# Kernel tuning notes

Measured on AMD Instinct MI355X. Metric: run time of the kernel, lower is better.

Reference implementation:

```python
import jax, jax.numpy as jnp
import numpy as np

B, S, E = 1, 2048, 2048
H = 16            # num_q_heads
DN = 128          # qk_nope_head_dim
DR = 64           # qk_rope_head_dim
DV = 128          # v_head_dim
R = 512           # kv_lora_rank
QLR = 1536        # q_lora_rank
EPS = 1e-6
ROPE_BASE = 10000.0


def _rmsnorm(x, w):
    var = jnp.mean(jnp.square(x), axis=-1, keepdims=True)
    return x * jax.lax.rsqrt(var + EPS) * w


def _rope_cos_sin(seqlen):
    inv_freq = 1.0 / (ROPE_BASE ** (jnp.arange(0, DR, 2, dtype=jnp.float32) / DR))
    ang = jnp.arange(seqlen, dtype=jnp.float32)[:, None] * inv_freq[None, :]  # [S, DR/2]
    cos = jnp.concatenate([jnp.cos(ang), jnp.cos(ang)], axis=-1)  # [S, DR]
    sin = jnp.concatenate([jnp.sin(ang), jnp.sin(ang)], axis=-1)
    return cos, sin


def _rotate_half(x):
    x1, x2 = jnp.split(x, 2, axis=-1)
    return jnp.concatenate([-x2, x1], axis=-1)


def setup_inputs() -> dict:
    key = jax.random.key(0)
    ks = jax.random.split(key, 8)
    sd = lambda fan_in: 1.0 / np.sqrt(fan_in)
    return {
        "x": jax.random.normal(ks[0], (B, S, E), jnp.float32),
        "w_q_a": jax.random.normal(ks[1], (E, QLR), jnp.float32) * sd(E),
        "q_a_ln_w": jnp.ones((QLR,), jnp.float32),
        "w_q_b": jax.random.normal(ks[2], (QLR, H * (DN + DR)), jnp.float32) * sd(QLR),
        "w_kv_a": jax.random.normal(ks[3], (E, R + DR), jnp.float32) * sd(E),
        "kv_a_ln_w": jnp.ones((R,), jnp.float32),
        "w_kv_b": jax.random.normal(ks[4], (R, H * (DN + DV)), jnp.float32) * sd(R),
        "w_o": jax.random.normal(ks[5], (H * DV, E), jnp.float32) * sd(H * DV),
    }


def reference(x, w_q_a, q_a_ln_w, w_q_b, w_kv_a, kv_a_ln_w, w_kv_b, w_o):
    b, s, _ = x.shape
    # --- low-rank query projection: q_a -> RMSNorm -> q_b ---
    q_a = _rmsnorm(x @ w_q_a, q_a_ln_w)                      # [b,s,QLR]
    q = (q_a @ w_q_b).reshape(b, s, H, DN + DR)               # [b,s,H,192]
    q_nope, q_pe = q[..., :DN], q[..., DN:]
    # --- compressed KV projection (MQA, single KV head) ---
    ckv_kpe = x @ w_kv_a                                      # [b,s,R+DR]
    ckv = _rmsnorm(ckv_kpe[..., :R], kv_a_ln_w)               # [b,s,R]
    k_pe = ckv_kpe[..., R:].reshape(b, s, 1, DR)              # [b,s,1,DR]
    # --- partial RoPE on the rope sub-dims only ---
    cos, sin = _rope_cos_sin(s)
    cos, sin = cos[None, :, None, :], sin[None, :, None, :]
    q_pe = q_pe * cos + _rotate_half(q_pe) * sin
    k_pe = k_pe * cos + _rotate_half(k_pe) * sin
    # --- weight absorption: fold W_uk into q, W_uv @ W_o into output ---
    w_kv = w_kv_b.reshape(R, H, DN + DV)
    w_uk = w_kv[..., :DN]                                     # [R,H,DN]
    w_uv = w_kv[..., DN:]                                     # [R,H,DV]
    w_o3 = w_o.reshape(H, DV, E)
    w_o_abs = jnp.einsum('rhd,hde->hre', w_uv, w_o3)          # [H,R,E]
    q_abs = jnp.einsum('bshd,rhd->bshr', q_nope, w_uk)        # [b,s,H,R]
    # --- attention in compressed (ckv + rope) space ---
    q_full = jnp.concatenate([q_abs, q_pe], axis=-1)          # [b,s,H,R+DR]
    k_full = jnp.concatenate([ckv, k_pe[:, :, 0, :]], axis=-1)  # [b,s,R+DR]
    sm_scale = (DN + DR) ** -0.5
    scores = jnp.einsum('bqhd,bkd->bhqk', q_full, k_full) * sm_scale
    causal = jnp.tril(jnp.ones((s, s), dtype=bool))
    scores = jnp.where(causal[None, None], scores, jnp.finfo(scores.dtype).min)
    attn = jax.nn.softmax(scores, axis=-1)
    o_ckv = jnp.einsum('bhqk,bkr->bqhr', attn, ckv)           # [b,s,H,R]
    # --- absorbed output projection, summed over heads ---
    y = jnp.einsum('bqhr,hre->bqe', o_ckv, w_o_abs)           # [b,s,E]
    return y
```

## Files before the change

### kernel.cpp

```cpp
#include <hip/hip_runtime.h>
#include <math.h>


typedef unsigned short u16;
typedef unsigned int u32;
typedef __bf16 bf16x8 __attribute__((ext_vector_type(8)));
typedef float f32x4 __attribute__((ext_vector_type(4)));

__device__ __forceinline__ u16 f2b(float f) {
  u32 u = __float_as_uint(f);
  u += 0x7FFFu + ((u >> 16) & 1u);
  return (u16)(u >> 16);
}
__device__ __forceinline__ float b2f(u16 v) {
  return __uint_as_float(((u32)v) << 16);
}

#define GLDS(g, l) __builtin_amdgcn_global_load_lds( \
    (const __attribute__((address_space(1))) u32*)(g), \
    (__attribute__((address_space(3))) u32*)(l), 16, 0, 0)

#define MFMA(a, b, c) __builtin_amdgcn_mfma_f32_16x16x32_bf16(a, b, c, 0, 0, 0)

template<int N>
__device__ __forceinline__ void vm_barrier() {
  __builtin_amdgcn_s_waitcnt(0xF70 | N);
  __builtin_amdgcn_s_barrier();
}

__device__ __forceinline__ float block_sum(float v, float* red) {
#pragma unroll
  for (int off = 32; off > 0; off >>= 1) v += __shfl_down(v, off);
  const int lane = threadIdx.x & 63, w = threadIdx.x >> 6;
  if (lane == 0) red[w] = v;
  __syncthreads();
  float r = red[0] + red[1] + red[2] + red[3];
  __syncthreads();
  return r;
}

template<int OUTK>
__global__ __launch_bounds__(256) void gemm_mfma(
    const u16* __restrict__ A, const u16* __restrict__ B, void* __restrict__ Cv,
    int K, int lda, int ldb, int ldc, long sA, long sB, long sC)
{
  __shared__ u16 At[3][4096];
  __shared__ u16 Bt[3][4096];
  const u16* Ab = A + (long)blockIdx.z * sA;
  const u16* Bb = B + (long)blockIdx.z * sB;
  const int tid = threadIdx.x;
  const int w = tid >> 6, lane = tid & 63;
  const int m0 = blockIdx.y * 128, n0 = blockIdx.x * 128;
  const int wm = (w >> 1) * 64, wn = (w & 1) * 64;
  const int fr = lane & 15, fq = lane >> 4;

  const int c0 = w * 2, c1 = w * 2 + 1;
  const int e0 = (c0 * 64 + lane) * 8, e1 = (c1 * 64 + lane) * 8;
  const int r0 = e0 >> 5, col0 = e0 & 31;
  const int r1 = e1 >> 5, col1 = e1 & 31;

  const int nk = K >> 5;
  auto issue = [&](int kc) {
    const int k0 = kc * 32;
    u16* at = At[kc % 3];
    u16* bt = Bt[kc % 3];
    GLDS(Ab + (long)(m0 + r0) * lda + k0 + col0, at + c0 * 512);
    GLDS(Bb + (long)(n0 + r0) * ldb + k0 + col0, bt + c0 * 512);
    GLDS(Ab + (long)(m0 + r1) * lda + k0 + col1, at + c1 * 512);
    GLDS(Bb + (long)(n0 + r1) * ldb + k0 + col1, bt + c1 * 512);
  };

  f32x4 acc[4][4] = {};
  issue(0);
  issue(1);
  vm_barrier<4>();
  for (int kc = 0; kc < nk; ++kc) {
    if (kc + 2 < nk) issue(kc + 2);
    const u16* at = At[kc % 3];
    const u16* bt = Bt[kc % 3];
    bf16x8 af[4], bfr[4];
#pragma unroll
    for (int i = 0; i < 4; ++i)
      af[i] = *(const bf16x8*)(at + (wm + i * 16 + fr) * 32 + fq * 8);
#pragma unroll
    for (int j = 0; j < 4; ++j)
      bfr[j] = *(const bf16x8*)(bt + (wn + j * 16 + fr) * 32 + fq * 8);
#pragma unroll
    for (int i = 0; i < 4; ++i)
#pragma unroll
      for (int j = 0; j < 4; ++j)
        acc[i][j] = MFMA(af[i], bfr[j], acc[i][j]);
    if (kc + 1 < nk) {
      if (kc + 2 < nk) vm_barrier<4>();
      else vm_barrier<0>();
    }
  }

  if (OUTK == 0) {
    float* C = (float*)Cv + (long)blockIdx.z * sC;
#pragma unroll
    for (int i = 0; i < 4; ++i)
#pragma unroll
      for (int j = 0; j < 4; ++j) {
        long base = (long)(m0 + wm + i * 16 + fq * 4) * ldc + (n0 + wn + j * 16 + fr);
#pragma unroll
        for (int r = 0; r < 4; ++r) C[base + (long)r * ldc] = acc[i][j][r];
      }
  } else if (OUTK == 1) {
    u16* C = (u16*)Cv + (long)blockIdx.z * sC;
#pragma unroll
    for (int i = 0; i < 4; ++i)
#pragma unroll
      for (int j = 0; j < 4; ++j) {
        long base = (long)(m0 + wm + i * 16 + fq * 4) * ldc + (n0 + wn + j * 16 + fr);
#pragma unroll
        for (int r = 0; r < 4; ++r) C[base + (long)r * ldc] = f2b(acc[i][j][r]);
      }
  } else {
    u16* C = (u16*)Cv + (long)blockIdx.z * sC;
#pragma unroll
    for (int i = 0; i < 4; ++i)
#pragma unroll
      for (int j = 0; j < 4; ++j) {
        ushort4 v = { f2b(acc[i][j][0]), f2b(acc[i][j][1]),
                      f2b(acc[i][j][2]), f2b(acc[i][j][3]) };
        *(ushort4*)(C + (long)(n0 + wn + j * 16 + fr) * ldc + (m0 + wm + i * 16 + fq * 4)) = v;
      }
  }
}

__global__ __launch_bounds__(256, 2) void attn_flash2(
    const u16* __restrict__ qfb,
    const u16* __restrict__ kfb,
    const u16* __restrict__ vallT,
    u16* __restrict__ ovb)
{
  __shared__ u16 Ks[3][4096];
  __shared__ u16 Vs[16384];
  __shared__ u16 Ps[4 * 2176];

  const int h = blockIdx.x;
  const int y = blockIdx.y;
  const int qt = (y & 1) ? (y >> 1) : (31 - (y >> 1));
  const int q0 = qt * 64;
  const int tid = threadIdx.x;
  const int w = tid >> 6, lane = tid & 63;
  const int fr = lane & 15, fq = lane >> 4;
  const float scale = 0.07216878364870323f;
  const int ktiles = (qt >> 1) + 1;
  u16* Psw = Ps + w * 2176;

  bf16x8 aq[18];
  {
    const u16* qp = qfb + (long)(q0 + w * 16 + fr) * 9216 + h * 576 + fq * 8;
#pragma unroll
    for (int d = 0; d < 18; ++d) aq[d] = *(const bf16x8*)(qp + d * 32);
  }

  const int krow0 = (w * 2) * 16 + (lane >> 2);
  const int krow1 = (w * 2 + 1) * 16 + (lane >> 2);
  const int kg0 = (lane & 3) ^ (krow0 & 3);
  const int kg1 = (lane & 3) ^ (krow1 & 3);
  const int vlanecol = lane >> 4;
  const int vslot = lane & 15;

  float m_run[4], l_run[4];
#pragma unroll
  for (int r = 0; r < 4; ++r) { m_run[r] = -1e30f; l_run[r] = 0.f; }
  f32x4 Oacc[8] = {};
  const u16* vbase = vallT + (long)h * 262144;

  for (int kt = 0; kt < ktiles; ++kt) {
    const int k0 = kt * 128;
    auto issueK = [&](int c) {
      const int d0 = c * 32;
      u16* dst = Ks[c % 3];
      GLDS(kfb + (long)(k0 + krow0) * 576 + d0 + kg0 * 8, dst + (w * 2) * 512);
      GLDS(kfb + (long)(k0 + krow1) * 576 + d0 + kg1 * 8, dst + (w * 2 + 1) * 512);
    };

    issueK(0);
    issueK(1);
    vm_barrier<2>();
    f32x4 sc[8] = {};
#pragma unroll
    for (int d = 0; d < 18; ++d) {
      if (d + 2 < 18) issueK(d + 2);
      const u16* kb = Ks[d % 3];
#pragma unroll
      for (int j = 0; j < 8; ++j) {
        const int row = j * 16 + fr;
        bf16x8 b = *(const bf16x8*)(kb + row * 32 + ((fq ^ (row & 3)) * 8));
        sc[j] = MFMA(aq[d], b, sc[j]);
      }
      if (d < 17) {
        if (d + 2 < 18) vm_barrier<2>();
        else vm_barrier<0>();
      }
    }

#pragma unroll
    for (int c = 0; c < 8; ++c) {
      const int i = w * 8 + c;
      const int vcol = i * 4 + vlanecol;
      const int g = vslot ^ (vcol & 15);
      GLDS(vbase + (long)vcol * 2048 + k0 + g * 8, Vs + i * 512);
    }

    const bool diag = (kt == ktiles - 1);
#pragma unroll
    for (int r = 0; r < 4; ++r) {
      float mx = m_run[r];
#pragma unroll
      for (int j = 0; j < 8; ++j) {
        float s = sc[j][r] * scale;
        if (diag) {
          const int row = q0 + w * 16 + fq * 4 + r;
          const int col = k0 + j * 16 + fr;
          if (col > row) s = -1e30f;
        }
        sc[j][r] = s;
        mx = fmaxf(mx, s);
      }
      mx = fmaxf(mx, __shfl_xor(mx, 1));
      mx = fmaxf(mx, __shfl_xor(mx, 2));
      mx = fmaxf(mx, __shfl_xor(mx, 4));
      mx = fmaxf(mx, __shfl_xor(mx, 8));
      const float alpha = __expf(m_run[r] - mx);
      m_run[r] = mx;
      float sum = 0.f;
#pragma unroll
      for (int j = 0; j < 8; ++j) {
        float p = __expf(sc[j][r] - mx);
        sc[j][r] = p;
        sum += p;
      }
      sum += __shfl_xor(sum, 1);
      sum += __shfl_xor(sum, 2);
      sum += __shfl_xor(sum, 4);
      sum += __shfl_xor(sum, 8);
      l_run[r] = l_run[r] * alpha + sum;
#pragma unroll
      for (int jv = 0; jv < 8; ++jv) Oacc[jv][r] *= alpha;
#pragma unroll
      for (int j = 0; j < 8; ++j)
        Psw[(fq * 4 + r) * 136 + j * 16 + fr] = f2b(sc[j][r]);
    }
    vm_barrier<0>();

#pragma unroll
    for (int ks = 0; ks < 4; ++ks) {
      bf16x8 ap = *(const bf16x8*)(Psw + fr * 136 + ks * 32 + fq * 8);
#pragma unroll
      for (int jv = 0; jv < 8; ++jv) {
        const int vcol = jv * 16 + fr;
        bf16x8 vb = *(const bf16x8*)(Vs + vcol * 128 + (((ks * 4 + fq) ^ fr) * 8));
        Oacc[jv] = MFMA(ap, vb, Oacc[jv]);
      }
    }
    __builtin_amdgcn_s_barrier();
  }

#pragma unroll
  for (int r = 0; r < 4; ++r) {
    const float inv = 1.0f / l_run[r];
    const long row = q0 + w * 16 + fq * 4 + r;
#pragma unroll
    for (int jv = 0; jv < 8; ++jv)
      ovb[row * 2048 + h * 128 + jv * 16 + fr] = f2b(Oacc[jv][r] * inv);
  }
}

__global__ __launch_bounds__(256) void cast_bf16(const float* __restrict__ in,
                                                 u16* __restrict__ out, long n) {
  long i = ((long)blockIdx.x * 256 + threadIdx.x) * 4;
  if (i >= n) return;
  float4 v = *(const float4*)(in + i);
  ushort4 o = { f2b(v.x), f2b(v.y), f2b(v.z), f2b(v.w) };
  *(ushort4*)(out + i) = o;
}

__global__ __launch_bounds__(256) void transpose_cast(const float* __restrict__ in,
    u16* __restrict__ out, int ldi, int ldo, long sIn, long sOut) {
  in += (long)blockIdx.z * sIn;
  out += (long)blockIdx.z * sOut;
  __shared__ u16 t[32][33];
  const int i0 = blockIdx.y * 32, j0 = blockIdx.x * 32;
  const int tx = threadIdx.x & 31, ty = threadIdx.x >> 5;
  for (int r = ty; r < 32; r += 8)
    t[r][tx] = f2b(in[(long)(i0 + r) * ldi + j0 + tx]);
  __syncthreads();
  for (int r = ty; r < 32; r += 8)
    out[(long)(j0 + r) * ldo + i0 + tx] = t[tx][r];
}

__global__ __launch_bounds__(256) void rmsnorm_cast(const float* __restrict__ in,
    const float* __restrict__ w, u16* __restrict__ out, int n) {
  __shared__ float red[4];
  const float* row = in + (long)blockIdx.x * n;
  u16* orow = out + (long)blockIdx.x * n;
  float ss = 0.f;
  for (int i = threadIdx.x; i < n; i += 256) { float v = row[i]; ss += v * v; }
  float tot = block_sum(ss, red);
  float inv = rsqrtf(tot / (float)n + 1e-6f);
  for (int i = threadIdx.x; i < n; i += 256) orow[i] = f2b(row[i] * inv * w[i]);
}

__global__ __launch_bounds__(256) void rope_table(float* tab) {
  int s = blockIdx.x * 8 + (threadIdx.x >> 5), j = threadIdx.x & 31;
  double freq = pow(10000.0, -(double)j / 32.0);
  double ang = (double)s * freq;
  tab[s * 64 + j] = (float)cos(ang);
  tab[s * 64 + 32 + j] = (float)sin(ang);
}

__global__ __launch_bounds__(256) void build_kfull(const float* __restrict__ ckv,
    const float* __restrict__ lnw, const float* __restrict__ tab, u16* __restrict__ kfb) {
  __shared__ float red[4];
  const int s = blockIdx.x;
  const float* row = ckv + (long)s * 640;
  float ss = 0.f;
  for (int i = threadIdx.x; i < 512; i += 256) { float v = row[i]; ss += v * v; }
  float tot = block_sum(ss, red);
  float inv = rsqrtf(tot / 512.0f + 1e-6f);
  u16* orow = kfb + (long)s * 576;
  for (int i = threadIdx.x; i < 512; i += 256) orow[i] = f2b(row[i] * inv * lnw[i]);
  if (threadIdx.x < 64) {
    int i = threadIdx.x, j = i & 31;
    float c = tab[s * 64 + j], sn = tab[s * 64 + 32 + j];
    float xv = row[512 + i];
    float rot = (i < 32) ? -row[512 + i + 32] : row[512 + i - 32];
    orow[512 + i] = f2b(xv * c + rot * sn);
  }
}

__global__ void rope_qpe(const u16* __restrict__ qb, const float* __restrict__ tab,
                         u16* __restrict__ qfb) {
  int s = blockIdx.x, h = blockIdx.y, i = threadIdx.x;
  int j = i & 31;
  float c = tab[s * 64 + j], sn = tab[s * 64 + 32 + j];
  const u16* src = qb + (long)s * 3072 + h * 192 + 128;
  float xv = b2f(src[i]);
  float rot = (i < 32) ? -b2f(src[i + 32]) : b2f(src[i - 32]);
  qfb[(long)s * 9216 + h * 576 + 512 + i] = f2b(xv * c + rot * sn);
}

extern "C" void kernel_launch(void* const* d_in, const int* in_sizes, int n_in,
                              void* d_out, int out_size, void* d_ws, size_t ws_size,
                              hipStream_t stream) {
  const float* x      = (const float*)d_in[0];
  const float* w_q_a  = (const float*)d_in[1];
  const float* q_ln   = (const float*)d_in[2];
  const float* w_q_b  = (const float*)d_in[3];
  const float* w_kv_a = (const float*)d_in[4];
  const float* kv_ln  = (const float*)d_in[5];
  const float* w_kv_b = (const float*)d_in[6];
  const float* w_o    = (const float*)d_in[7];
  float* out = (float*)d_out;

  char* p = (char*)d_ws;
  float* tab   = (float*)p;  p += 524288;
  u16* wkvbb   = (u16*)p;    p += 4194304;
  u16* wuvT    = (u16*)p;    p += 2097152;
  u16* woT     = (u16*)p;    p += 8388608;
  u16* qfb     = (u16*)p;    p += 37748736;
  u16* vallT   = (u16*)p;    p += 8388608;
  u16* kfb     = (u16*)p;    p += 2359296;
  u16* ovb     = (u16*)p;    p += 8388608;
  char* tb = p;
  u16* xb      = (u16*)tb;
  u16* wqaT    = (u16*)(tb + 8388608);
  float* qa    = (float*)(tb + 14680064);
  u16* qab     = (u16*)(tb + 27262976);
  u16* wqbT    = (u16*)(tb + 33554432);
  u16* qb      = (u16*)(tb + 42991616);
  u16* wkvaT   = (u16*)(tb + 55574528);
  float* ckv   = (float*)(tb + 58195968);

  rope_table<<<dim3(256), 256, 0, stream>>>(tab);

  cast_bf16<<<4096, 256, 0, stream>>>(x, xb, 4194304);
  transpose_cast<<<dim3(48, 64), 256, 0, stream>>>(w_q_a, wqaT, 1536, 2048, 0, 0);
  transpose_cast<<<dim3(96, 48), 256, 0, stream>>>(w_q_b, wqbT, 3072, 1536, 0, 0);
  transpose_cast<<<dim3(18, 64), 256, 0, stream>>>(w_kv_a, wkvaT, 576, 2048, 0, 0);
  cast_bf16<<<2048, 256, 0, stream>>>(w_kv_b, wkvbb, 2097152);
  transpose_cast<<<dim3(4, 16, 16), 256, 0, stream>>>(w_kv_b + 128, wuvT, 4096, 512, 256, 65536);
  transpose_cast<<<dim3(64, 64), 256, 0, stream>>>(w_o, woT, 2048, 2048, 0, 0);

  gemm_mfma<0><<<dim3(12, 16), 256, 0, stream>>>(
      xb, wqaT, qa, 2048, 2048, 2048, 1536, 0, 0, 0);
  rmsnorm_cast<<<2048, 256, 0, stream>>>(qa, q_ln, qab, 1536);

  gemm_mfma<1><<<dim3(24, 16), 256, 0, stream>>>(
      qab, wqbT, qb, 1536, 1536, 1536, 3072, 0, 0, 0);

  gemm_mfma<0><<<dim3(5, 16), 256, 0, stream>>>(
      xb, wkvaT, ckv, 2048, 2048, 2048, 640, 0, 0, 0);
  build_kfull<<<2048, 256, 0, stream>>>(ckv, kv_ln, tab, kfb);

  gemm_mfma<1><<<dim3(4, 16, 16), 256, 0, stream>>>(
      qb, wkvbb, qfb, 128, 3072, 4096, 9216, 192, 256, 576);
  rope_qpe<<<dim3(2048, 16), 64, 0, stream>>>(qb, tab, qfb);

  gemm_mfma<2><<<dim3(1, 16, 16), 256, 0, stream>>>(
      kfb, wuvT, vallT, 512, 576, 512, 2048, 0, 65536, 262144);

  attn_flash2<<<dim3(16, 32), 256, 0, stream>>>(qfb, kfb, vallT, ovb);

  gemm_mfma<0><<<dim3(16, 16), 256, 0, stream>>>(
      ovb, woT, out, 2048, 2048, 2048, 2048, 0, 0, 0);
}
```

Before: 547.8 us.

## Split attention into KV chunks with atomic work queue plus reduce; fuse q_a/kv_a GEMMs

Attention is split into work items of at most four KV tiles per (q tile, head). A persistent grid of 512 blocks pulls these items from an atomic counter, longest-first, and writes unnormalised partial outputs and (max, sum) stats. A separate reduce kernel merges the partials. This targets the load imbalance from causal masking in the old one-block-per-qtile launch, at the cost of extra partial-buffer traffic and an extra kernel. The x@w_q_a and x@w_kv_a GEMMs are also merged into one wider GEMM, and rope_qpe is repacked to 256 threads per row, cutting launches.

```diff
diff --git a/kernel.cpp b/kernel.cpp
--- a/kernel.cpp
+++ b/kernel.cpp
@@ -6,6 +6,7 @@
 typedef unsigned int u32;
 typedef __bf16 bf16x8 __attribute__((ext_vector_type(8)));
 typedef float f32x4 __attribute__((ext_vector_type(4)));
+typedef unsigned short u16x8 __attribute__((ext_vector_type(8)));
 
 __device__ __forceinline__ u16 f2b(float f) {
   u32 u = __float_as_uint(f);
@@ -27,6 +28,9 @@
   __builtin_amdgcn_s_waitcnt(0xF70 | N);
   __builtin_amdgcn_s_barrier();
 }
+
+#define N_ITEMS 1280
+__device__ __forceinline__ int nkc_of(int qt) { return (((qt >> 1) + 1) + 3) >> 2; }
 
 __device__ __forceinline__ float block_sum(float v, float* red) {
 #pragma unroll
@@ -129,33 +133,26 @@
   }
 }
 
-__global__ __launch_bounds__(256, 2) void attn_flash2(
+__global__ void init_ctr(u32* ctr) { *ctr = 0; }
+
+__global__ __launch_bounds__(256, 2) void attn_partial(
     const u16* __restrict__ qfb,
     const u16* __restrict__ kfb,
     const u16* __restrict__ vallT,
-    u16* __restrict__ ovb)
+    u32* __restrict__ ctr,
+    u16* __restrict__ pO,
+    float* __restrict__ pS)
 {
   __shared__ u16 Ks[3][4096];
   __shared__ u16 Vs[16384];
   __shared__ u16 Ps[4 * 2176];
-
-  const int h = blockIdx.x;
-  const int y = blockIdx.y;
-  const int qt = (y & 1) ? (y >> 1) : (31 - (y >> 1));
-  const int q0 = qt * 64;
+  __shared__ u32 cur;
+
   const int tid = threadIdx.x;
   const int w = tid >> 6, lane = tid & 63;
   const int fr = lane & 15, fq = lane >> 4;
   const float scale = 0.07216878364870323f;
-  const int ktiles = (qt >> 1) + 1;
   u16* Psw = Ps + w * 2176;
-
-  bf16x8 aq[18];
-  {
-    const u16* qp = qfb + (long)(q0 + w * 16 + fr) * 9216 + h * 576 + fq * 8;
-#pragma unroll
-    for (int d = 0; d < 18; ++d) aq[d] = *(const bf16x8*)(qp + d * 32);
-  }
 
   const int krow0 = (w * 2) * 16 + (lane >> 2);
   const int krow1 = (w * 2 + 1) * 16 + (lane >> 2);
@@ -164,110 +161,177 @@
   const int vlanecol = lane >> 4;
   const int vslot = lane & 15;
 
-  float m_run[4], l_run[4];
-#pragma unroll
-  for (int r = 0; r < 4; ++r) { m_run[r] = -1e30f; l_run[r] = 0.f; }
-  f32x4 Oacc[8] = {};
-  const u16* vbase = vallT + (long)h * 262144;
-
-  for (int kt = 0; kt < ktiles; ++kt) {
-    const int k0 = kt * 128;
-    auto issueK = [&](int c) {
-      const int d0 = c * 32;
-      u16* dst = Ks[c % 3];
-      GLDS(kfb + (long)(k0 + krow0) * 576 + d0 + kg0 * 8, dst + (w * 2) * 512);
-      GLDS(kfb + (long)(k0 + krow1) * 576 + d0 + kg1 * 8, dst + (w * 2 + 1) * 512);
-    };
-
-    issueK(0);
-    issueK(1);
-    vm_barrier<2>();
-    f32x4 sc[8] = {};
-#pragma unroll
-    for (int d = 0; d < 18; ++d) {
-      if (d + 2 < 18) issueK(d + 2);
-      const u16* kb = Ks[d % 3];
-#pragma unroll
-      for (int j = 0; j < 8; ++j) {
-        const int row = j * 16 + fr;
-        bf16x8 b = *(const bf16x8*)(kb + row * 32 + ((fq ^ (row & 3)) * 8));
-        sc[j] = MFMA(aq[d], b, sc[j]);
-      }
-      if (d < 17) {
-        if (d + 2 < 18) vm_barrier<2>();
-        else vm_barrier<0>();
-      }
-    }
-
-#pragma unroll
-    for (int c = 0; c < 8; ++c) {
-      const int i = w * 8 + c;
-      const int vcol = i * 4 + vlanecol;
-      const int g = vslot ^ (vcol & 15);
-      GLDS(vbase + (long)vcol * 2048 + k0 + g * 8, Vs + i * 512);
-    }
-
-    const bool diag = (kt == ktiles - 1);
+  while (true) {
+    if (tid == 0) cur = atomicAdd(ctr, 1u);
+    __syncthreads();
+    const u32 it = cur;
+    if (it >= N_ITEMS) break;
+
+    int rem = (int)it, qt = 31, kc = 0, h = 0;
+    for (int q = 31; q >= 0; --q) {
+      int cnt = nkc_of(q) * 16;
+      if (rem < cnt) { qt = q; kc = rem >> 4; h = rem & 15; break; }
+      rem -= cnt;
+    }
+    const int q0 = qt * 64;
+    const int ktt = (qt >> 1) + 1;
+    const int kt0 = kc * 4, kt1 = min(kt0 + 4, ktt);
+
+    bf16x8 aq[18];
+    {
+      const u16* qp = qfb + (long)(q0 + w * 16 + fr) * 9216 + h * 576 + fq * 8;
+#pragma unroll
+      for (int d = 0; d < 18; ++d) aq[d] = *(const bf16x8*)(qp + d * 32);
+    }
+
+    float m_run[4], l_run[4];
+#pragma unroll
+    for (int r = 0; r < 4; ++r) { m_run[r] = -1e30f; l_run[r] = 0.f; }
+    f32x4 Oacc[8] = {};
+    const u16* vbase = vallT + (long)h * 262144;
+
+    for (int kt = kt0; kt < kt1; ++kt) {
+      const int k0 = kt * 128;
+      auto issueK = [&](int c) {
+        const int d0 = c * 32;
+        u16* dst = Ks[c % 3];
+        GLDS(kfb + (long)(k0 + krow0) * 576 + d0 + kg0 * 8, dst + (w * 2) * 512);
+        GLDS(kfb + (long)(k0 + krow1) * 576 + d0 + kg1 * 8, dst + (w * 2 + 1) * 512);
+      };
+
+      issueK(0);
+      issueK(1);
+      vm_barrier<2>();
+      f32x4 sc[8] = {};
+#pragma unroll
+      for (int d = 0; d < 18; ++d) {
+        if (d + 2 < 18) issueK(d + 2);
+        const u16* kb = Ks[d % 3];
+#pragma unroll
+        for (int j = 0; j < 8; ++j) {
+          const int row = j * 16 + fr;
+          bf16x8 b = *(const bf16x8*)(kb + row * 32 + ((fq ^ (row & 3)) * 8));
+          sc[j] = MFMA(aq[d], b, sc[j]);
+        }
+        if (d < 17) {
+          if (d + 2 < 18) vm_barrier<2>();
+          else vm_barrier<0>();
+        }
+      }
+
+#pragma unroll
+      for (int c = 0; c < 8; ++c) {
+        const int i = w * 8 + c;
+        const int vcol = i * 4 + vlanecol;
+        const int g = vslot ^ (vcol & 15);
+        GLDS(vbase + (long)vcol * 2048 + k0 + g * 8, Vs + i * 512);
+      }
+
+      const bool diag = (kt == ktt - 1);
+#pragma unroll
+      for (int r = 0; r < 4; ++r) {
+        float mx = m_run[r];
+#pragma unroll
+        for (int j = 0; j < 8; ++j) {
+          float s = sc[j][r] * scale;
+          if (diag) {
+            const int row = q0 + w * 16 + fq * 4 + r;
+            const int col = k0 + j * 16 + fr;
+            if (col > row) s = -1e30f;
+          }
+          sc[j][r] = s;
+          mx = fmaxf(mx, s);
+        }
+        mx = fmaxf(mx, __shfl_xor(mx, 1));
+        mx = fmaxf(mx, __shfl_xor(mx, 2));
+        mx = fmaxf(mx, __shfl_xor(mx, 4));
+        mx = fmaxf(mx, __shfl_xor(mx, 8));
+        const float alpha = __expf(m_run[r] - mx);
+        m_run[r] = mx;
+        float sum = 0.f;
+#pragma unroll
+        for (int j = 0; j < 8; ++j) {
+          float p = __expf(sc[j][r] - mx);
+          sc[j][r] = p;
+          sum += p;
+        }
+        sum += __shfl_xor(sum, 1);
+        sum += __shfl_xor(sum, 2);
+        sum += __shfl_xor(sum, 4);
+        sum += __shfl_xor(sum, 8);
+        l_run[r] = l_run[r] * alpha + sum;
+#pragma unroll
+        for (int jv = 0; jv < 8; ++jv) Oacc[jv][r] *= alpha;
+#pragma unroll
+        for (int j = 0; j < 8; ++j)
+          Psw[(fq * 4 + r) * 136 + j * 16 + fr] = f2b(sc[j][r]);
+      }
+      vm_barrier<0>();
+
+#pragma unroll
+      for (int ks = 0; ks < 4; ++ks) {
+        bf16x8 ap = *(const bf16x8*)(Psw + fr * 136 + ks * 32 + fq * 8);
+#pragma unroll
+        for (int jv = 0; jv < 8; ++jv) {
+          const int vcol = jv * 16 + fr;
+          bf16x8 vb = *(const bf16x8*)(Vs + vcol * 128 + (((ks * 4 + fq) ^ fr) * 8));
+          Oacc[jv] = MFMA(ap, vb, Oacc[jv]);
+        }
+      }
+      __builtin_amdgcn_s_barrier();
+    }
+
+    const long po = (long)it * 8192;
 #pragma unroll
     for (int r = 0; r < 4; ++r) {
-      float mx = m_run[r];
-#pragma unroll
-      for (int j = 0; j < 8; ++j) {
-        float s = sc[j][r] * scale;
-        if (diag) {
-          const int row = q0 + w * 16 + fq * 4 + r;
-          const int col = k0 + j * 16 + fr;
-          if (col > row) s = -1e30f;
-        }
-        sc[j][r] = s;
-        mx = fmaxf(mx, s);
-      }
-      mx = fmaxf(mx, __shfl_xor(mx, 1));
-      mx = fmaxf(mx, __shfl_xor(mx, 2));
-      mx = fmaxf(mx, __shfl_xor(mx, 4));
-      mx = fmaxf(mx, __shfl_xor(mx, 8));
-      const float alpha = __expf(m_run[r] - mx);
-      m_run[r] = mx;
-      float sum = 0.f;
-#pragma unroll
-      for (int j = 0; j < 8; ++j) {
-        float p = __expf(sc[j][r] - mx);
-        sc[j][r] = p;
-        sum += p;
-      }
-      sum += __shfl_xor(sum, 1);
-      sum += __shfl_xor(sum, 2);
-      sum += __shfl_xor(sum, 4);
-      sum += __shfl_xor(sum, 8);
-      l_run[r] = l_run[r] * alpha + sum;
-#pragma unroll
-      for (int jv = 0; jv < 8; ++jv) Oacc[jv][r] *= alpha;
-#pragma unroll
-      for (int j = 0; j < 8; ++j)
-        Psw[(fq * 4 + r) * 136 + j * 16 + fr] = f2b(sc[j][r]);
-    }
-    vm_barrier<0>();
-
-#pragma unroll
-    for (int ks = 0; ks < 4; ++ks) {
-      bf16x8 ap = *(const bf16x8*)(Psw + fr * 136 + ks * 32 + fq * 8);
-#pragma unroll
-      for (int jv = 0; jv < 8; ++jv) {
-        const int vcol = jv * 16 + fr;
-        bf16x8 vb = *(const bf16x8*)(Vs + vcol * 128 + (((ks * 4 + fq) ^ fr) * 8));
-        Oacc[jv] = MFMA(ap, vb, Oacc[jv]);
-      }
-    }
-    __builtin_amdgcn_s_barrier();
-  }
-
-#pragma unroll
-  for (int r = 0; r < 4; ++r) {
-    const float inv = 1.0f / l_run[r];
-    const long row = q0 + w * 16 + fq * 4 + r;
-#pragma unroll
-    for (int jv = 0; jv < 8; ++jv)
-      ovb[row * 2048 + h * 128 + jv * 16 + fr] = f2b(Oacc[jv][r] * inv);
+      const int lr = w * 16 + fq * 4 + r;
+      if (fr == 0) {
+        pS[((long)it * 64 + lr) * 2] = m_run[r];
+        pS[((long)it * 64 + lr) * 2 + 1] = l_run[r];
+      }
+#pragma unroll
+      for (int jv = 0; jv < 8; ++jv)
+        pO[po + (long)lr * 128 + jv * 16 + fr] = f2b(Oacc[jv][r]);
+    }
+  }
+}
+
+__global__ __launch_bounds__(256) void attn_reduce(
+    const u16* __restrict__ pO, const float* __restrict__ pS,
+    u16* __restrict__ ovb)
+{
+  const int h = blockIdx.x, qt = blockIdx.y;
+  const int ktt = (qt >> 1) + 1;
+  const int nkc = (ktt + 3) >> 2;
+  int base = 0;
+  for (int q = qt + 1; q < 32; ++q) base += nkc_of(q) * 16;
+  const int tid = threadIdx.x;
+  const int r = tid >> 2, cq = (tid & 3) * 32;
+
+  float m[4], l[4], wgt[4];
+  float M = -1e30f;
+  for (int i = 0; i < nkc; ++i) {
+    const long slot = base + i * 16 + h;
+    m[i] = pS[(slot * 64 + r) * 2];
+    l[i] = pS[(slot * 64 + r) * 2 + 1];
+    M = fmaxf(M, m[i]);
+  }
+  float L = 0.f;
+  for (int i = 0; i < nkc; ++i) { wgt[i] = __expf(m[i] - M); L += l[i] * wgt[i]; }
+  const float inv = 1.0f / L;
+
+  u16* orow = ovb + (long)(qt * 64 + r) * 2048 + h * 128 + cq;
+  for (int c8 = 0; c8 < 32; c8 += 8) {
+    float acc[8] = {};
+    for (int i = 0; i < nkc; ++i) {
+      const u16x8 v = *(const u16x8*)(pO + ((long)(base + i * 16 + h) * 64 + r) * 128 + cq + c8);
+#pragma unroll
+      for (int e = 0; e < 8; ++e) acc[e] += b2f(v[e]) * wgt[i];
+    }
+    u16x8 o;
+#pragma unroll
+    for (int e = 0; e < 8; ++e) o[e] = f2b(acc[e] * inv);
+    *(u16x8*)(orow + c8) = o;
   }
 }
 
@@ -295,9 +359,9 @@
 }
 
 __global__ __launch_bounds__(256) void rmsnorm_cast(const float* __restrict__ in,
-    const float* __restrict__ w, u16* __restrict__ out, int n) {
+    const float* __restrict__ w, u16* __restrict__ out, int n, int ldin) {
   __shared__ float red[4];
-  const float* row = in + (long)blockIdx.x * n;
+  const float* row = in + (long)blockIdx.x * ldin;
   u16* orow = out + (long)blockIdx.x * n;
   float ss = 0.f;
   for (int i = threadIdx.x; i < n; i += 256) { float v = row[i]; ss += v * v; }
@@ -318,7 +382,7 @@
     const float* __restrict__ lnw, const float* __restrict__ tab, u16* __restrict__ kfb) {
   __shared__ float red[4];
   const int s = blockIdx.x;
-  const float* row = ckv + (long)s * 640;
+  const float* row = ckv + (long)s * 2176;
   float ss = 0.f;
   for (int i = threadIdx.x; i < 512; i += 256) { float v = row[i]; ss += v * v; }
   float tot = block_sum(ss, red);
@@ -334,15 +398,21 @@
   }
 }
 
-__global__ void rope_qpe(const u16* __restrict__ qb, const float* __restrict__ tab,
-                         u16* __restrict__ qfb) {
-  int s = blockIdx.x, h = blockIdx.y, i = threadIdx.x;
-  int j = i & 31;
-  float c = tab[s * 64 + j], sn = tab[s * 64 + 32 + j];
+__global__ __launch_bounds__(256) void rope_qpe(const u16* __restrict__ qb,
+    const float* __restrict__ tab, u16* __restrict__ qfb) {
+  const int s = blockIdx.x;
+  const int h = threadIdx.x >> 4;
+  const int i0 = (threadIdx.x & 15) * 4;
   const u16* src = qb + (long)s * 3072 + h * 192 + 128;
-  float xv = b2f(src[i]);
-  float rot = (i < 32) ? -b2f(src[i + 32]) : b2f(src[i - 32]);
-  qfb[(long)s * 9216 + h * 576 + 512 + i] = f2b(xv * c + rot * sn);
+  u16* dst = qfb + (long)s * 9216 + h * 576 + 512;
+#pragma unroll
+  for (int k = 0; k < 4; ++k) {
+    const int i = i0 + k, j = i & 31;
+    float c = tab[s * 64 + j], sn = tab[s * 64 + 32 + j];
+    float xv = b2f(src[i]);
+    float rot = (i < 32) ? -b2f(src[i + 32]) : b2f(src[i - 32]);
+    dst[i] = f2b(xv * c + rot * sn);
+  }
 }
 
 extern "C" void kernel_launch(void* const* d_in, const int* in_sizes, int n_in,
@@ -369,43 +439,43 @@
   u16* ovb     = (u16*)p;    p += 8388608;
   char* tb = p;
   u16* xb      = (u16*)tb;
-  u16* wqaT    = (u16*)(tb + 8388608);
-  float* qa    = (float*)(tb + 14680064);
-  u16* qab     = (u16*)(tb + 27262976);
-  u16* wqbT    = (u16*)(tb + 33554432);
-  u16* qb      = (u16*)(tb + 42991616);
-  u16* wkvaT   = (u16*)(tb + 55574528);
-  float* ckv   = (float*)(tb + 58195968);
+  u16* wabT    = (u16*)(tb + 8388608);
+  float* qac   = (float*)(tb + 17301504);
+  u16* qab     = (u16*)(tb + 35127296);
+  u16* wqbT    = (u16*)(tb + 41418752);
+  u16* qb      = (u16*)(tb + 50855936);
+  u16* pO      = (u16*)tb;
+  float* pS    = (float*)(tb + 20971520);
+  u32* ctr     = (u32*)(tb + 21626880);
 
   rope_table<<<dim3(256), 256, 0, stream>>>(tab);
 
   cast_bf16<<<4096, 256, 0, stream>>>(x, xb, 4194304);
-  transpose_cast<<<dim3(48, 64), 256, 0, stream>>>(w_q_a, wqaT, 1536, 2048, 0, 0);
+  transpose_cast<<<dim3(48, 64), 256, 0, stream>>>(w_q_a, wabT, 1536, 2048, 0, 0);
+  transpose_cast<<<dim3(18, 64), 256, 0, stream>>>(w_kv_a, wabT + 1536 * 2048, 576, 2048, 0, 0);
   transpose_cast<<<dim3(96, 48), 256, 0, stream>>>(w_q_b, wqbT, 3072, 1536, 0, 0);
-  transpose_cast<<<dim3(18, 64), 256, 0, stream>>>(w_kv_a, wkvaT, 576, 2048, 0, 0);
   cast_bf16<<<2048, 256, 0, stream>>>(w_kv_b, wkvbb, 2097152);
   transpose_cast<<<dim3(4, 16, 16), 256, 0, stream>>>(w_kv_b + 128, wuvT, 4096, 512, 256, 65536);
   transpose_cast<<<dim3(64, 64), 256, 0, stream>>>(w_o, woT, 2048, 2048, 0, 0);
 
-  gemm_mfma<0><<<dim3(12, 16), 256, 0, stream>>>(
-      xb, wqaT, qa, 2048, 2048, 2048, 1536, 0, 0, 0);
-  rmsnorm_cast<<<2048, 256, 0, stream>>>(qa, q_ln, qab, 1536);
+  gemm_mfma<0><<<dim3(17, 16), 256, 0, stream>>>(
+      xb, wabT, qac, 2048, 2048, 2048, 2176, 0, 0, 0);
+  rmsnorm_cast<<<2048, 256, 0, stream>>>(qac, q_ln, qab, 1536, 2176);
+  build_kfull<<<2048, 256, 0, stream>>>(qac + 1536, kv_ln, tab, kfb);
 
   gemm_mfma<1><<<dim3(24, 16), 256, 0, stream>>>(
       qab, wqbT, qb, 1536, 1536, 1536, 3072, 0, 0, 0);
 
-  gemm_mfma<0><<<dim3(5, 16), 256, 0, stream>>>(
-      xb, wkvaT, ckv, 2048, 2048, 2048, 640, 0, 0, 0);
-  build_kfull<<<2048, 256, 0, stream>>>(ckv, kv_ln, tab, kfb);
-
   gemm_mfma<1><<<dim3(4, 16, 16), 256, 0, stream>>>(
       qb, wkvbb, qfb, 128, 3072, 4096, 9216, 192, 256, 576);
-  rope_qpe<<<dim3(2048, 16), 64, 0, stream>>>(qb, tab, qfb);
+  rope_qpe<<<dim3(2048), 256, 0, stream>>>(qb, tab, qfb);
 
   gemm_mfma<2><<<dim3(1, 16, 16), 256, 0, stream>>>(
       kfb, wuvT, vallT, 512, 576, 512, 2048, 0, 65536, 262144);
 
-  attn_flash2<<<dim3(16, 32), 256, 0, stream>>>(qfb, kfb, vallT, ovb);
+  init_ctr<<<1, 1, 0, stream>>>(ctr);
+  attn_partial<<<dim3(512), 256, 0, stream>>>(qfb, kfb, vallT, ctr, pO, pS);
+  attn_reduce<<<dim3(16, 32), 256, 0, stream>>>(pO, pS, ovb);
 
   gemm_mfma<0><<<dim3(16, 16), 256, 0, stream>>>(
       ovb, woT, out, 2048, 2048, 2048, 2048, 0, 0, 0);
```

New measurement: 477.1 us. 12.9% less time.
